# Kernel tuning notes

Hardware: AMD Instinct MI355X
Metric: run time of the kernel (lower is better)

Reference implementation:

```python
import jax, jax.numpy as jnp
import numpy as np

N_NODES = 50000
N_EDGES = 625000
D = 128


def setup_inputs() -> dict:
    key = jax.random.key(0)
    kx, ks, kr, kw, kb = jax.random.split(key, 5)
    x = jax.random.normal(kx, (N_NODES, D), dtype=jnp.float32)
    senders = jax.random.randint(ks, (N_EDGES,), 0, N_NODES, dtype=jnp.int64)
    receivers = jax.random.randint(kr, (N_EDGES,), 0, N_NODES, dtype=jnp.int64)
    # nn.Linear(2*D, D): weight [D, 2*D], bias [D]
    lim = 1.0 / np.sqrt(2 * D)
    W = jax.random.uniform(kw, (D, 2 * D), minval=-lim, maxval=lim, dtype=jnp.float32)
    b = jax.random.uniform(kb, (D,), minval=-lim, maxval=lim, dtype=jnp.float32)
    return {"x": x, "senders": senders, "receivers": receivers, "n_nodes": N_NODES, "W": W, "b": b}


def reference(x, senders, receivers, n_nodes, W, b):
    # Add self loops (with_self=True)
    self_idx = jnp.arange(n_nodes, dtype=senders.dtype)
    s = jnp.concatenate([senders, self_idx])   # [E + N]
    r = jnp.concatenate([receivers, self_idx]) # [E + N]

    ones = jnp.ones(r.shape[0], dtype=x.dtype)
    # degree_norm=True branch (note: mirrors the original's naming exactly:
    # 'out_degree' counted over receivers, 'in_degree' over senders)
    out_degree = jax.ops.segment_sum(ones, r, num_segments=n_nodes)  # [N]
    in_degree = jax.ops.segment_sum(ones, s, num_segments=n_nodes)   # [N]
    out_degree_norm = jax.lax.rsqrt(jnp.maximum(out_degree, 1.0))
    in_degree_norm = jax.lax.rsqrt(jnp.maximum(in_degree, 1.0))

    # Gather sender embeddings, scale, scatter-add to receivers
    sender_emb = x[s] * out_degree_norm[s][:, None]  # [E+N, D]
    aggregated = jax.ops.segment_sum(sender_emb, r, num_segments=n_nodes)  # [N, D]

    # edge_count over receivers == out_degree (same scatter), clamped
    edge_count = jnp.maximum(out_degree, 1.0)
    aggregated = aggregated / edge_count[:, None]
    aggregated = aggregated * in_degree_norm[:, None]

    combined = jnp.concatenate([x, aggregated], axis=1)  # [N, 2D]
    return combined @ W.T + b
```

## Files before the change

kernel.cpp:

```cpp
#include <hip/hip_runtime.h>

#define DIM 128
#define BM 128
#define BK 32
#define BINSZ 128
#define EPB 2048

typedef __attribute__((ext_vector_type(8))) short short8;
typedef __attribute__((ext_vector_type(4))) float f32x4;

__device__ __forceinline__ unsigned short f2bf(float f) {
    unsigned int b = __float_as_uint(f);
    return (unsigned short)((b + 0x7fffu + ((b >> 16) & 1u)) >> 16);
}
__device__ __forceinline__ float bf_lo(unsigned int u) { return __uint_as_float(u << 16); }
__device__ __forceinline__ float bf_hi(unsigned int u) { return __uint_as_float(u & 0xffff0000u); }
__device__ __forceinline__ unsigned int pack2(float a, float b) {
    return (unsigned int)f2bf(a) | ((unsigned int)f2bf(b) << 16);
}
__device__ __forceinline__ uint2 pack4(float4 v) {
    uint2 r; r.x = pack2(v.x, v.y); r.y = pack2(v.z, v.w); return r;
}

__global__ __launch_bounds__(256) void hist_kernel(
        const int* __restrict__ senders, const int* __restrict__ receivers,
        const float4* __restrict__ W4, uint2* __restrict__ Wb4,
        int* __restrict__ Hr, int* __restrict__ Hs, int E, int nbin, int nw4) {
    __shared__ int hr[512], hs[512];
    int t = threadIdx.x;

    int gi = blockIdx.x * 256 + t;
    if (gi < nw4) Wb4[gi] = pack4(W4[gi]);

    for (int b = t; b < nbin; b += 256) { hr[b] = 0; hs[b] = 0; }
    __syncthreads();
    int base = blockIdx.x * EPB;
    for (int k = 0; k < EPB; k += 256) {
        int e = base + k + t;
        if (e < E) {
            atomicAdd(&hr[receivers[e] >> 7], 1);
            atomicAdd(&hs[senders[e] >> 7], 1);
        }
    }
    __syncthreads();
    size_t ho = (size_t)blockIdx.x * nbin;
    for (int b = t; b < nbin; b += 256) {
        Hr[ho + b] = hr[b];
        Hs[ho + b] = hs[b];
    }
}

__global__ __launch_bounds__(512) void scan_bins_kernel(
        int* __restrict__ Hr, int* __restrict__ Hs,
        int* __restrict__ tot_r, int* __restrict__ tot_s,
        int NAB, int nbin) {
    __shared__ int sr[512], ss[512];
    int b = blockIdx.x, t = threadIdx.x;
    int vr = (t < NAB) ? Hr[(size_t)t * nbin + b] : 0;
    int vs = (t < NAB) ? Hs[(size_t)t * nbin + b] : 0;
    sr[t] = vr; ss[t] = vs;
    __syncthreads();
    for (int off = 1; off < 512; off <<= 1) {
        int ur = (t >= off) ? sr[t - off] : 0;
        int us = (t >= off) ? ss[t - off] : 0;
        __syncthreads();
        sr[t] += ur; ss[t] += us;
        __syncthreads();
    }
    if (t < NAB) {
        Hr[(size_t)t * nbin + b] = sr[t] - vr;
        Hs[(size_t)t * nbin + b] = ss[t] - vs;
    }
    if (t == 511) { tot_r[b] = sr[511]; tot_s[b] = ss[511]; }
}

__global__ __launch_bounds__(512) void scan_base_kernel(
        const int* __restrict__ tot_r, const int* __restrict__ tot_s,
        int* __restrict__ base_r, int* __restrict__ base_s,
        int* __restrict__ row_start, int nbin, int N, int E) {
    __shared__ int sr[512], ss[512];
    int t = threadIdx.x;
    int vr = (t < nbin) ? tot_r[t] : 0;
    int vs = (t < nbin) ? tot_s[t] : 0;
    sr[t] = vr; ss[t] = vs;
    __syncthreads();
    for (int off = 1; off < 512; off <<= 1) {
        int ur = (t >= off) ? sr[t - off] : 0;
        int us = (t >= off) ? ss[t - off] : 0;
        __syncthreads();
        sr[t] += ur; ss[t] += us;
        __syncthreads();
    }
    if (t < nbin) {
        base_r[t] = sr[t] - vr;
        base_s[t] = ss[t] - vs;
    }
    if (t == 0) { base_r[nbin] = E; base_s[nbin] = E; row_start[N] = E; }
}

__global__ __launch_bounds__(256) void scatter_kernel(
        const int* __restrict__ senders, const int* __restrict__ receivers,
        const int* __restrict__ Hr, const int* __restrict__ Hs,
        const int* __restrict__ base_r, const int* __restrict__ base_s,
        unsigned int* __restrict__ bucket_r, int* __restrict__ bucket_s,
        int E, int nbin) {
    __shared__ int br_[512], bs_[512];
    int t = threadIdx.x;
    size_t ho = (size_t)blockIdx.x * nbin;
    for (int b = t; b < nbin; b += 256) {
        br_[b] = base_r[b] + Hr[ho + b];
        bs_[b] = base_s[b] + Hs[ho + b];
    }
    __syncthreads();
    int base = blockIdx.x * EPB;
    for (int k = 0; k < EPB; k += 256) {
        int e = base + k + t;
        if (e < E) {
            int s = senders[e], r = receivers[e];
            int pr = atomicAdd(&br_[r >> 7], 1);
            bucket_r[pr] = ((unsigned int)(r & 127) << 16) | (unsigned int)s;
            int ps = atomicAdd(&bs_[s >> 7], 1);
            bucket_s[ps] = s;
        }
    }
}

__global__ __launch_bounds__(256) void fine_kernel(
        const unsigned int* __restrict__ bucket_r,
        const int* __restrict__ bucket_s,
        const int* __restrict__ base_r,
        const int* __restrict__ base_s,
        const float4* __restrict__ x4,
        uint2* __restrict__ xb2,
        int* __restrict__ edge_src,
        int* __restrict__ row_start,
        float* __restrict__ fs,
        uint2* __restrict__ xs2,
        int N) {
    __shared__ int fine[BINSZ], fstart[BINSZ], cs[BINSZ];
    __shared__ float scs[BINSZ];
    int b = blockIdx.x, t = threadIdx.x;
    if (t < BINSZ) { fine[t] = 0; cs[t] = 0; }
    __syncthreads();

    int loR = base_r[b], hiR = base_r[b + 1];
    int loS = base_s[b], hiS = base_s[b + 1];
    for (int i = loR + t; i < hiR; i += 256)
        atomicAdd(&fine[bucket_r[i] >> 16], 1);
    for (int i = loS + t; i < hiS; i += 256)
        atomicAdd(&cs[bucket_s[i] & 127], 1);
    __syncthreads();

    if (t < BINSZ) fstart[t] = fine[t];
    __syncthreads();
    for (int off = 1; off < BINSZ; off <<= 1) {
        int u = (t < BINSZ && t >= off) ? fstart[t - off] : 0;
        __syncthreads();
        if (t < BINSZ) fstart[t] += u;
        __syncthreads();
    }
    if (t < BINSZ) {
        int excl = fstart[t] - fine[t];
        int node = b * BINSZ + t;
        float od = (float)(fine[t] + 1);
        float sc = rsqrtf(od);
        scs[t] = sc;
        if (node < N) {
            row_start[node] = loR + excl;
            fs[node] = rsqrtf((float)(cs[t] + 1)) / od;
        }
        fstart[t] = excl;
    }
    __syncthreads();

    for (int i = loR + t; i < hiR; i += 256) {
        unsigned int u = bucket_r[i];
        int pos = atomicAdd(&fstart[u >> 16], 1);
        edge_src[loR + pos] = (int)(u & 0xFFFFu);
    }

    int nrow0 = b * BINSZ;
    for (int idx = t; idx < BINSZ * 32; idx += 256) {
        int row = idx >> 5, c = idx & 31;
        int node = nrow0 + row;
        if (node < N) {
            float4 v = x4[(size_t)node * 32 + c];
            float sc = scs[row];
            xb2[(size_t)node * 32 + c] = pack4(v);
            float4 vs;
            vs.x = v.x * sc; vs.y = v.y * sc; vs.z = v.z * sc; vs.w = v.w * sc;
            xs2[(size_t)node * 32 + c] = pack4(vs);
        }
    }
}

__global__ __launch_bounds__(256) void gather_kernel(
        const uint4* __restrict__ xs4,
        const int* __restrict__ edge_src,
        const int* __restrict__ row_start,
        const float* __restrict__ fs,
        uint4* __restrict__ aggb4,
        int N) {
    int lane = threadIdx.x & 63;
    int grp  = lane >> 4;
    int gl   = lane & 15;
    int wid  = (blockIdx.x * blockDim.x + threadIdx.x) >> 6;
    int n    = wid * 4 + grp;
    bool valid = (n < N);

    int start = 0, deg = 0;
    if (valid) {
        start = row_start[n];
        deg   = row_start[n + 1] - start;
    }
    int md = deg;
    md = max(md, __shfl_xor(md, 16));
    md = max(md, __shfl_xor(md, 32));

    float a[8];
#pragma unroll
    for (int q = 0; q < 8; q++) a[q] = 0.f;

    for (int base = 0; base < md; base += 16) {
        int e = base + gl;
        int src = -1;
        if (e < deg) src = edge_src[start + e];
#pragma unroll
        for (int j = 0; j < 16; j++) {
            int s = __shfl(src, (grp << 4) | j);
            if (s >= 0) {
                uint4 u = xs4[(size_t)s * 16 + gl];
                a[0] += bf_lo(u.x); a[1] += bf_hi(u.x);
                a[2] += bf_lo(u.y); a[3] += bf_hi(u.y);
                a[4] += bf_lo(u.z); a[5] += bf_hi(u.z);
                a[6] += bf_lo(u.w); a[7] += bf_hi(u.w);
            }
        }
    }

    if (valid) {
        float f = fs[n];
        uint4 u = xs4[(size_t)n * 16 + gl];
        a[0] = (a[0] + bf_lo(u.x)) * f; a[1] = (a[1] + bf_hi(u.x)) * f;
        a[2] = (a[2] + bf_lo(u.y)) * f; a[3] = (a[3] + bf_hi(u.y)) * f;
        a[4] = (a[4] + bf_lo(u.z)) * f; a[5] = (a[5] + bf_hi(u.z)) * f;
        a[6] = (a[6] + bf_lo(u.w)) * f; a[7] = (a[7] + bf_hi(u.w)) * f;
        uint4 o;
        o.x = pack2(a[0], a[1]); o.y = pack2(a[2], a[3]);
        o.z = pack2(a[4], a[5]); o.w = pack2(a[6], a[7]);
        aggb4[(size_t)n * 16 + gl] = o;
    }
}

__global__ __launch_bounds__(512) void gemm_kernel(
        const unsigned short* __restrict__ x_bf,
        const unsigned short* __restrict__ agg_bf,
        const unsigned short* __restrict__ W_bf,
        const float* __restrict__ bias,
        float* __restrict__ out, int N) {
    __shared__ unsigned short As[BM * BK];
    __shared__ unsigned short Bs[DIM * BK];

    int t    = threadIdx.x;
    int lane = t & 63;
    int w    = t >> 6;
    int wr   = w >> 2, wc = w & 3;
    int row0 = blockIdx.x * BM;

    f32x4 acc[4][2];
#pragma unroll
    for (int i = 0; i < 4; i++)
#pragma unroll
        for (int j = 0; j < 2; j++) acc[i][j] = (f32x4){0.f, 0.f, 0.f, 0.f};

    for (int kt = 0; kt < 8; kt++) {
        const unsigned short* src = (kt < 4) ? x_bf : agg_bf;
        int k0 = (kt & 3) * BK;
        {
            int row = t >> 2, ch = t & 3;
            uint4 v = *(const uint4*)&src[(size_t)(row0 + row) * 128 + k0 + ch * 8];
            *(uint4*)&As[row * BK + ch * 8] = v;
        }
        {
            int n = t >> 2, ch = t & 3;
            uint4 v = *(const uint4*)&W_bf[(size_t)n * 256 + kt * BK + ch * 8];
            *(uint4*)&Bs[n * BK + ch * 8] = v;
        }
        __syncthreads();

        short8 a[4], b[2];
#pragma unroll
        for (int i = 0; i < 4; i++)
            a[i] = *(const short8*)&As[(wr * 64 + i * 16 + (lane & 15)) * BK + (lane >> 4) * 8];
#pragma unroll
        for (int j = 0; j < 2; j++)
            b[j] = *(const short8*)&Bs[(wc * 32 + j * 16 + (lane & 15)) * BK + (lane >> 4) * 8];
#pragma unroll
        for (int i = 0; i < 4; i++)
#pragma unroll
            for (int j = 0; j < 2; j++)
                acc[i][j] = __builtin_amdgcn_mfma_f32_16x16x32_bf16(a[i], b[j], acc[i][j], 0, 0, 0);
        __syncthreads();
    }

    int cq = lane >> 4;
    int cl = lane & 15;
#pragma unroll
    for (int j = 0; j < 2; j++) {
        int col = wc * 32 + j * 16 + cl;
        float bb = bias[col];
#pragma unroll
        for (int i = 0; i < 4; i++) {
            int rbase = row0 + wr * 64 + i * 16 + cq * 4;
#pragma unroll
            for (int r = 0; r < 4; r++) {
                int row = rbase + r;
                if (row < N) out[(size_t)row * DIM + col] = acc[i][j][r] + bb;
            }
        }
    }
}

extern "C" void kernel_launch(void* const* d_in, const int* in_sizes, int n_in,
                              void* d_out, int out_size, void* d_ws, size_t ws_size,
                              hipStream_t stream) {
    const float* x         = (const float*)d_in[0];
    const int*   senders   = (const int*)d_in[1];
    const int*   receivers = (const int*)d_in[2];
    const float* W         = (const float*)d_in[4];
    const float* bias      = (const float*)d_in[5];
    float*       out       = (float*)d_out;

    int N    = in_sizes[0] / DIM;
    int E    = in_sizes[1];
    int nbin = (N + BINSZ - 1) / BINSZ;
    int NAB  = (E + EPB - 1) / EPB;
    int NP   = ((N + BM - 1) / BM) * BM;

    char* ws = (char*)d_ws;
    size_t off = 0;
    #define WS_ALLOC(ptrtype, name, bytes) \
        ptrtype name = (ptrtype)(ws + off); off += (((size_t)(bytes)) + 255) & ~(size_t)255;
    WS_ALLOC(int*,            tot_r,     (size_t)nbin * 4)
    WS_ALLOC(int*,            tot_s,     (size_t)nbin * 4)
    WS_ALLOC(int*,            base_r,    (size_t)(nbin + 1) * 4)
    WS_ALLOC(int*,            base_s,    (size_t)(nbin + 1) * 4)
    WS_ALLOC(int*,            row_start, (size_t)(N + 1) * 4)
    WS_ALLOC(float*,          fs,        (size_t)N * 4)
    WS_ALLOC(int*,            edge_src,  (size_t)E * 4)
    WS_ALLOC(unsigned short*, x_bf,      (size_t)NP * DIM * 2)
    WS_ALLOC(unsigned short*, xs_bf,     (size_t)NP * DIM * 2)
    WS_ALLOC(unsigned short*, agg_bf,    (size_t)NP * DIM * 2)
    WS_ALLOC(unsigned short*, W_bf,      (size_t)DIM * 256 * 2)
    #undef WS_ALLOC

    size_t eb = ((size_t)E * 4 + 255) & ~(size_t)255;
    size_t hb = ((size_t)NAB * nbin * 4 + 255) & ~(size_t)255;
    unsigned int* bucket_r = (unsigned int*)agg_bf;
    int*          bucket_s = (int*)((char*)agg_bf + eb);
    int*          Hr       = (int*)((char*)agg_bf + 2 * eb);
    int*          Hs       = (int*)((char*)agg_bf + 2 * eb + hb);

    int nw4 = DIM * 256 / 4;

    hist_kernel<<<NAB, 256, 0, stream>>>(senders, receivers,
                                         (const float4*)W, (uint2*)W_bf,
                                         Hr, Hs, E, nbin, nw4);
    scan_bins_kernel<<<nbin, 512, 0, stream>>>(Hr, Hs, tot_r, tot_s, NAB, nbin);
    scan_base_kernel<<<1, 512, 0, stream>>>(tot_r, tot_s, base_r, base_s,
                                            row_start, nbin, N, E);
    scatter_kernel<<<NAB, 256, 0, stream>>>(senders, receivers, Hr, Hs,
                                            base_r, base_s, bucket_r, bucket_s, E, nbin);
    fine_kernel<<<nbin, 256, 0, stream>>>(bucket_r, bucket_s, base_r, base_s,
                                          (const float4*)x, (uint2*)x_bf,
                                          edge_src, row_start, fs,
                                          (uint2*)xs_bf, N);
    int nwave = (N + 3) / 4;
    gather_kernel<<<(nwave * 64 + 255) / 256, 256, 0, stream>>>(
        (const uint4*)xs_bf, edge_src, row_start, fs,
        (uint4*)agg_bf, N);
    gemm_kernel<<<(N + BM - 1) / BM, 512, 0, stream>>>(
        x_bf, agg_bf, W_bf, bias, out, N);
}
```

Before: 176.5 us.

## Fuse neighbor gather into GEMM and count sender degree with global atomics

```diff
diff --git a/kernel.cpp b/kernel.cpp
--- a/kernel.cpp
+++ b/kernel.cpp
@@ -23,94 +23,73 @@
 }
 
 __global__ __launch_bounds__(256) void hist_kernel(
-        const int* __restrict__ senders, const int* __restrict__ receivers,
+        const int* __restrict__ receivers,
         const float4* __restrict__ W4, uint2* __restrict__ Wb4,
-        int* __restrict__ Hr, int* __restrict__ Hs, int E, int nbin, int nw4) {
-    __shared__ int hr[512], hs[512];
+        int* __restrict__ Hr, int* __restrict__ deg_s,
+        int E, int nbin, int nw4, int N) {
+    __shared__ int hr[512];
     int t = threadIdx.x;
 
     int gi = blockIdx.x * 256 + t;
     if (gi < nw4) Wb4[gi] = pack4(W4[gi]);
-
-    for (int b = t; b < nbin; b += 256) { hr[b] = 0; hs[b] = 0; }
+    for (int i = gi; i < N; i += gridDim.x * 256) deg_s[i] = 0;
+
+    for (int b = t; b < nbin; b += 256) hr[b] = 0;
     __syncthreads();
     int base = blockIdx.x * EPB;
     for (int k = 0; k < EPB; k += 256) {
         int e = base + k + t;
-        if (e < E) {
-            atomicAdd(&hr[receivers[e] >> 7], 1);
-            atomicAdd(&hs[senders[e] >> 7], 1);
-        }
+        if (e < E) atomicAdd(&hr[receivers[e] >> 7], 1);
     }
     __syncthreads();
     size_t ho = (size_t)blockIdx.x * nbin;
-    for (int b = t; b < nbin; b += 256) {
-        Hr[ho + b] = hr[b];
-        Hs[ho + b] = hs[b];
-    }
+    for (int b = t; b < nbin; b += 256) Hr[ho + b] = hr[b];
 }
 
 __global__ __launch_bounds__(512) void scan_bins_kernel(
-        int* __restrict__ Hr, int* __restrict__ Hs,
-        int* __restrict__ tot_r, int* __restrict__ tot_s,
-        int NAB, int nbin) {
-    __shared__ int sr[512], ss[512];
+        int* __restrict__ Hr, int* __restrict__ tot_r, int NAB, int nbin) {
+    __shared__ int sr[512];
     int b = blockIdx.x, t = threadIdx.x;
     int vr = (t < NAB) ? Hr[(size_t)t * nbin + b] : 0;
-    int vs = (t < NAB) ? Hs[(size_t)t * nbin + b] : 0;
-    sr[t] = vr; ss[t] = vs;
+    sr[t] = vr;
     __syncthreads();
     for (int off = 1; off < 512; off <<= 1) {
         int ur = (t >= off) ? sr[t - off] : 0;
-        int us = (t >= off) ? ss[t - off] : 0;
-        __syncthreads();
-        sr[t] += ur; ss[t] += us;
-        __syncthreads();
-    }
-    if (t < NAB) {
-        Hr[(size_t)t * nbin + b] = sr[t] - vr;
-        Hs[(size_t)t * nbin + b] = ss[t] - vs;
-    }
-    if (t == 511) { tot_r[b] = sr[511]; tot_s[b] = ss[511]; }
+        __syncthreads();
+        sr[t] += ur;
+        __syncthreads();
+    }
+    if (t < NAB) Hr[(size_t)t * nbin + b] = sr[t] - vr;
+    if (t == 511) tot_r[b] = sr[511];
 }
 
 __global__ __launch_bounds__(512) void scan_base_kernel(
-        const int* __restrict__ tot_r, const int* __restrict__ tot_s,
-        int* __restrict__ base_r, int* __restrict__ base_s,
+        const int* __restrict__ tot_r, int* __restrict__ base_r,
         int* __restrict__ row_start, int nbin, int N, int E) {
-    __shared__ int sr[512], ss[512];
+    __shared__ int sr[512];
     int t = threadIdx.x;
     int vr = (t < nbin) ? tot_r[t] : 0;
-    int vs = (t < nbin) ? tot_s[t] : 0;
-    sr[t] = vr; ss[t] = vs;
+    sr[t] = vr;
     __syncthreads();
     for (int off = 1; off < 512; off <<= 1) {
         int ur = (t >= off) ? sr[t - off] : 0;
-        int us = (t >= off) ? ss[t - off] : 0;
-        __syncthreads();
-        sr[t] += ur; ss[t] += us;
-        __syncthreads();
-    }
-    if (t < nbin) {
-        base_r[t] = sr[t] - vr;
-        base_s[t] = ss[t] - vs;
-    }
-    if (t == 0) { base_r[nbin] = E; base_s[nbin] = E; row_start[N] = E; }
+        __syncthreads();
+        sr[t] += ur;
+        __syncthreads();
+    }
+    if (t < nbin) base_r[t] = sr[t] - vr;
+    if (t == 0) { base_r[nbin] = E; row_start[N] = E; }
 }
 
 __global__ __launch_bounds__(256) void scatter_kernel(
         const int* __restrict__ senders, const int* __restrict__ receivers,
-        const int* __restrict__ Hr, const int* __restrict__ Hs,
-        const int* __restrict__ base_r, const int* __restrict__ base_s,
-        unsigned int* __restrict__ bucket_r, int* __restrict__ bucket_s,
+        const int* __restrict__ Hr, const int* __restrict__ base_r,
+        unsigned int* __restrict__ bucket_r, int* __restrict__ deg_s,
         int E, int nbin) {
-    __shared__ int br_[512], bs_[512];
+    __shared__ int br_[512];
     int t = threadIdx.x;
     size_t ho = (size_t)blockIdx.x * nbin;
-    for (int b = t; b < nbin; b += 256) {
-        br_[b] = base_r[b] + Hr[ho + b];
-        bs_[b] = base_s[b] + Hs[ho + b];
-    }
+    for (int b = t; b < nbin; b += 256) br_[b] = base_r[b] + Hr[ho + b];
     __syncthreads();
     int base = blockIdx.x * EPB;
     for (int k = 0; k < EPB; k += 256) {
@@ -119,36 +98,30 @@
             int s = senders[e], r = receivers[e];
             int pr = atomicAdd(&br_[r >> 7], 1);
             bucket_r[pr] = ((unsigned int)(r & 127) << 16) | (unsigned int)s;
-            int ps = atomicAdd(&bs_[s >> 7], 1);
-            bucket_s[ps] = s;
+            atomicAdd(&deg_s[s], 1);
         }
     }
 }
 
 __global__ __launch_bounds__(256) void fine_kernel(
         const unsigned int* __restrict__ bucket_r,
-        const int* __restrict__ bucket_s,
         const int* __restrict__ base_r,
-        const int* __restrict__ base_s,
+        const int* __restrict__ deg_s,
         const float4* __restrict__ x4,
         uint2* __restrict__ xb2,
         int* __restrict__ edge_src,
         int* __restrict__ row_start,
         float* __restrict__ fs,
-        uint2* __restrict__ xs2,
+        float* __restrict__ sc,
         int N) {
-    __shared__ int fine[BINSZ], fstart[BINSZ], cs[BINSZ];
-    __shared__ float scs[BINSZ];
+    __shared__ int fine[BINSZ], fstart[BINSZ];
     int b = blockIdx.x, t = threadIdx.x;
-    if (t < BINSZ) { fine[t] = 0; cs[t] = 0; }
+    if (t < BINSZ) fine[t] = 0;
     __syncthreads();
 
     int loR = base_r[b], hiR = base_r[b + 1];
-    int loS = base_s[b], hiS = base_s[b + 1];
     for (int i = loR + t; i < hiR; i += 256)
         atomicAdd(&fine[bucket_r[i] >> 16], 1);
-    for (int i = loS + t; i < hiS; i += 256)
-        atomicAdd(&cs[bucket_s[i] & 127], 1);
     __syncthreads();
 
     if (t < BINSZ) fstart[t] = fine[t];
@@ -162,12 +135,11 @@
     if (t < BINSZ) {
         int excl = fstart[t] - fine[t];
         int node = b * BINSZ + t;
-        float od = (float)(fine[t] + 1);
-        float sc = rsqrtf(od);
-        scs[t] = sc;
         if (node < N) {
+            float od = (float)(fine[t] + 1);
             row_start[node] = loR + excl;
-            fs[node] = rsqrtf((float)(cs[t] + 1)) / od;
+            sc[node] = rsqrtf(od);
+            fs[node] = rsqrtf((float)(deg_s[node] + 1)) / od;
         }
         fstart[t] = excl;
     }
@@ -183,89 +155,88 @@
     for (int idx = t; idx < BINSZ * 32; idx += 256) {
         int row = idx >> 5, c = idx & 31;
         int node = nrow0 + row;
-        if (node < N) {
-            float4 v = x4[(size_t)node * 32 + c];
-            float sc = scs[row];
-            xb2[(size_t)node * 32 + c] = pack4(v);
-            float4 vs;
-            vs.x = v.x * sc; vs.y = v.y * sc; vs.z = v.z * sc; vs.w = v.w * sc;
-            xs2[(size_t)node * 32 + c] = pack4(vs);
-        }
-    }
-}
-
-__global__ __launch_bounds__(256) void gather_kernel(
-        const uint4* __restrict__ xs4,
+        if (node < N) xb2[(size_t)node * 32 + c] = pack4(x4[(size_t)node * 32 + c]);
+    }
+}
+
+__global__ __launch_bounds__(512) void gemm_kernel(
+        const unsigned short* __restrict__ x_bf,
         const int* __restrict__ edge_src,
         const int* __restrict__ row_start,
         const float* __restrict__ fs,
-        uint4* __restrict__ aggb4,
-        int N) {
-    int lane = threadIdx.x & 63;
-    int grp  = lane >> 4;
-    int gl   = lane & 15;
-    int wid  = (blockIdx.x * blockDim.x + threadIdx.x) >> 6;
-    int n    = wid * 4 + grp;
-    bool valid = (n < N);
-
-    int start = 0, deg = 0;
-    if (valid) {
-        start = row_start[n];
-        deg   = row_start[n + 1] - start;
-    }
-    int md = deg;
-    md = max(md, __shfl_xor(md, 16));
-    md = max(md, __shfl_xor(md, 32));
-
-    float a[8];
-#pragma unroll
-    for (int q = 0; q < 8; q++) a[q] = 0.f;
-
-    for (int base = 0; base < md; base += 16) {
-        int e = base + gl;
-        int src = -1;
-        if (e < deg) src = edge_src[start + e];
-#pragma unroll
-        for (int j = 0; j < 16; j++) {
-            int s = __shfl(src, (grp << 4) | j);
-            if (s >= 0) {
-                uint4 u = xs4[(size_t)s * 16 + gl];
-                a[0] += bf_lo(u.x); a[1] += bf_hi(u.x);
-                a[2] += bf_lo(u.y); a[3] += bf_hi(u.y);
-                a[4] += bf_lo(u.z); a[5] += bf_hi(u.z);
-                a[6] += bf_lo(u.w); a[7] += bf_hi(u.w);
-            }
-        }
-    }
-
-    if (valid) {
-        float f = fs[n];
-        uint4 u = xs4[(size_t)n * 16 + gl];
-        a[0] = (a[0] + bf_lo(u.x)) * f; a[1] = (a[1] + bf_hi(u.x)) * f;
-        a[2] = (a[2] + bf_lo(u.y)) * f; a[3] = (a[3] + bf_hi(u.y)) * f;
-        a[4] = (a[4] + bf_lo(u.z)) * f; a[5] = (a[5] + bf_hi(u.z)) * f;
-        a[6] = (a[6] + bf_lo(u.w)) * f; a[7] = (a[7] + bf_hi(u.w)) * f;
-        uint4 o;
-        o.x = pack2(a[0], a[1]); o.y = pack2(a[2], a[3]);
-        o.z = pack2(a[4], a[5]); o.w = pack2(a[6], a[7]);
-        aggb4[(size_t)n * 16 + gl] = o;
-    }
-}
-
-__global__ __launch_bounds__(512) void gemm_kernel(
-        const unsigned short* __restrict__ x_bf,
-        const unsigned short* __restrict__ agg_bf,
+        const float* __restrict__ sc,
         const unsigned short* __restrict__ W_bf,
         const float* __restrict__ bias,
         float* __restrict__ out, int N) {
     __shared__ unsigned short As[BM * BK];
     __shared__ unsigned short Bs[DIM * BK];
+    __shared__ unsigned short Agg[BM][136];
 
     int t    = threadIdx.x;
     int lane = t & 63;
     int w    = t >> 6;
     int wr   = w >> 2, wc = w & 3;
     int row0 = blockIdx.x * BM;
+    const uint4* xb4 = (const uint4*)x_bf;
+
+    {
+        int grp = lane >> 4;
+        int gl  = lane & 15;
+        for (int it = 0; it < 4; ++it) {
+            int nl = it * 32 + w * 4 + grp;
+            int n  = row0 + nl;
+            bool valid = (n < N);
+            int start = 0, deg = 0;
+            if (valid) { start = row_start[n]; deg = row_start[n + 1] - start; }
+            int md = deg;
+            md = max(md, __shfl_xor(md, 16));
+            md = max(md, __shfl_xor(md, 32));
+
+            float a[8];
+#pragma unroll
+            for (int q = 0; q < 8; q++) a[q] = 0.f;
+
+            for (int base = 0; base < md; base += 16) {
+                int e = base + gl;
+                int src = -1; float scv = 0.f;
+                if (e < deg) { src = edge_src[start + e]; scv = sc[src]; }
+#pragma unroll
+                for (int j = 0; j < 16; j++) {
+                    int   s  = __shfl(src, (grp << 4) | j);
+                    float sj = __shfl(scv, (grp << 4) | j);
+                    if (s >= 0) {
+                        uint4 u = xb4[(size_t)s * 16 + gl];
+                        a[0] = fmaf(sj, bf_lo(u.x), a[0]);
+                        a[1] = fmaf(sj, bf_hi(u.x), a[1]);
+                        a[2] = fmaf(sj, bf_lo(u.y), a[2]);
+                        a[3] = fmaf(sj, bf_hi(u.y), a[3]);
+                        a[4] = fmaf(sj, bf_lo(u.z), a[4]);
+                        a[5] = fmaf(sj, bf_hi(u.z), a[5]);
+                        a[6] = fmaf(sj, bf_lo(u.w), a[6]);
+                        a[7] = fmaf(sj, bf_hi(u.w), a[7]);
+                    }
+                }
+            }
+
+            uint4 o = make_uint4(0u, 0u, 0u, 0u);
+            if (valid) {
+                float f = fs[n], scn = sc[n];
+                uint4 u = xb4[(size_t)n * 16 + gl];
+                a[0] = (a[0] + bf_lo(u.x) * scn) * f;
+                a[1] = (a[1] + bf_hi(u.x) * scn) * f;
+                a[2] = (a[2] + bf_lo(u.y) * scn) * f;
+                a[3] = (a[3] + bf_hi(u.y) * scn) * f;
+                a[4] = (a[4] + bf_lo(u.z) * scn) * f;
+                a[5] = (a[5] + bf_hi(u.z) * scn) * f;
+                a[6] = (a[6] + bf_lo(u.w) * scn) * f;
+                a[7] = (a[7] + bf_hi(u.w) * scn) * f;
+                o.x = pack2(a[0], a[1]); o.y = pack2(a[2], a[3]);
+                o.z = pack2(a[4], a[5]); o.w = pack2(a[6], a[7]);
+            }
+            *(uint4*)&Agg[nl][gl * 8] = o;
+        }
+    }
+    __syncthreads();
 
     f32x4 acc[4][2];
 #pragma unroll
@@ -274,11 +245,10 @@
         for (int j = 0; j < 2; j++) acc[i][j] = (f32x4){0.f, 0.f, 0.f, 0.f};
 
     for (int kt = 0; kt < 8; kt++) {
-        const unsigned short* src = (kt < 4) ? x_bf : agg_bf;
         int k0 = (kt & 3) * BK;
-        {
+        if (kt < 4) {
             int row = t >> 2, ch = t & 3;
-            uint4 v = *(const uint4*)&src[(size_t)(row0 + row) * 128 + k0 + ch * 8];
+            uint4 v = *(const uint4*)&x_bf[(size_t)(row0 + row) * 128 + k0 + ch * 8];
             *(uint4*)&As[row * BK + ch * 8] = v;
         }
         {
@@ -289,9 +259,15 @@
         __syncthreads();
 
         short8 a[4], b[2];
-#pragma unroll
-        for (int i = 0; i < 4; i++)
-            a[i] = *(const short8*)&As[(wr * 64 + i * 16 + (lane & 15)) * BK + (lane >> 4) * 8];
+        if (kt < 4) {
+#pragma unroll
+            for (int i = 0; i < 4; i++)
+                a[i] = *(const short8*)&As[(wr * 64 + i * 16 + (lane & 15)) * BK + (lane >> 4) * 8];
+        } else {
+#pragma unroll
+            for (int i = 0; i < 4; i++)
+                a[i] = *(const short8*)&Agg[wr * 64 + i * 16 + (lane & 15)][k0 + (lane >> 4) * 8];
+        }
 #pragma unroll
         for (int j = 0; j < 2; j++)
             b[j] = *(const short8*)&Bs[(wc * 32 + j * 16 + (lane & 15)) * BK + (lane >> 4) * 8];
@@ -342,43 +318,30 @@
     #define WS_ALLOC(ptrtype, name, bytes) \
         ptrtype name = (ptrtype)(ws + off); off += (((size_t)(bytes)) + 255) & ~(size_t)255;
     WS_ALLOC(int*,            tot_r,     (size_t)nbin * 4)
-    WS_ALLOC(int*,            tot_s,     (size_t)nbin * 4)
     WS_ALLOC(int*,            base_r,    (size_t)(nbin + 1) * 4)
-    WS_ALLOC(int*,            base_s,    (size_t)(nbin + 1) * 4)
     WS_ALLOC(int*,            row_start, (size_t)(N + 1) * 4)
     WS_ALLOC(float*,          fs,        (size_t)N * 4)
+    WS_ALLOC(float*,          sc,        (size_t)N * 4)
+    WS_ALLOC(int*,            deg_s,     (size_t)N * 4)
     WS_ALLOC(int*,            edge_src,  (size_t)E * 4)
     WS_ALLOC(unsigned short*, x_bf,      (size_t)NP * DIM * 2)
-    WS_ALLOC(unsigned short*, xs_bf,     (size_t)NP * DIM * 2)
-    WS_ALLOC(unsigned short*, agg_bf,    (size_t)NP * DIM * 2)
     WS_ALLOC(unsigned short*, W_bf,      (size_t)DIM * 256 * 2)
+    WS_ALLOC(unsigned int*,   bucket_r,  (size_t)E * 4)
+    WS_ALLOC(int*,            Hr,        (size_t)NAB * nbin * 4)
     #undef WS_ALLOC
 
-    size_t eb = ((size_t)E * 4 + 255) & ~(size_t)255;
-    size_t hb = ((size_t)NAB * nbin * 4 + 255) & ~(size_t)255;
-    unsigned int* bucket_r = (unsigned int*)agg_bf;
-    int*          bucket_s = (int*)((char*)agg_bf + eb);
-    int*          Hr       = (int*)((char*)agg_bf + 2 * eb);
-    int*          Hs       = (int*)((char*)agg_bf + 2 * eb + hb);
-
     int nw4 = DIM * 256 / 4;
 
-    hist_kernel<<<NAB, 256, 0, stream>>>(senders, receivers,
+    hist_kernel<<<NAB, 256, 0, stream>>>(receivers,
                                          (const float4*)W, (uint2*)W_bf,
-                                         Hr, Hs, E, nbin, nw4);
-    scan_bins_kernel<<<nbin, 512, 0, stream>>>(Hr, Hs, tot_r, tot_s, NAB, nbin);
-    scan_base_kernel<<<1, 512, 0, stream>>>(tot_r, tot_s, base_r, base_s,
-                                            row_start, nbin, N, E);
-    scatter_kernel<<<NAB, 256, 0, stream>>>(senders, receivers, Hr, Hs,
-                                            base_r, base_s, bucket_r, bucket_s, E, nbin);
-    fine_kernel<<<nbin, 256, 0, stream>>>(bucket_r, bucket_s, base_r, base_s,
+                                         Hr, deg_s, E, nbin, nw4, N);
+    scan_bins_kernel<<<nbin, 512, 0, stream>>>(Hr, tot_r, NAB, nbin);
+    scan_base_kernel<<<1, 512, 0, stream>>>(tot_r, base_r, row_start, nbin, N, E);
+    scatter_kernel<<<NAB, 256, 0, stream>>>(senders, receivers, Hr, base_r,
+                                            bucket_r, deg_s, E, nbin);
+    fine_kernel<<<nbin, 256, 0, stream>>>(bucket_r, base_r, deg_s,
                                           (const float4*)x, (uint2*)x_bf,
-                                          edge_src, row_start, fs,
-                                          (uint2*)xs_bf, N);
-    int nwave = (N + 3) / 4;
-    gather_kernel<<<(nwave * 64 + 255) / 256, 256, 0, stream>>>(
-        (const uint4*)xs_bf, edge_src, row_start, fs,
-        (uint4*)agg_bf, N);
+                                          edge_src, row_start, fs, sc, N);
     gemm_kernel<<<(N + BM - 1) / BM, 512, 0, stream>>>(
-        x_bf, agg_bf, W_bf, bias, out, N);
-}
+        x_bf, edge_src, row_start, fs, sc, W_bf, bias, out, N);
+}
```

Result: slower. 196.3 us (+11.2%).
